# Kernel tuning notes

Measured on AMD Instinct MI355X. Metric: run time of the kernel, lower is better.

## Reference

```python
import jax, jax.numpy as jnp
import numpy as np

N = 8192
F_IN = 512
F_HID = 256
ALPHA = 0.2  # LeakyReLU negative slope
NEG_INF = -9e15


def gat_layer(h, adj, W, a):
    """Standard dense GraphAttentionLayer (pyGAT style).
    h: [N, F_in], adj: [N, N] (0/1), W: [F_in, F_out], a: [2*F_out, 1].
    """
    Wh = h @ W  # [N, F_out]
    f_out = W.shape[1]
    # e_ij = leakyrelu(a1 . Wh_i + a2 . Wh_j) via broadcasting
    e1 = Wh @ a[:f_out]      # [N, 1]
    e2 = Wh @ a[f_out:]      # [N, 1]
    e = jax.nn.leaky_relu(e1 + e2.T, negative_slope=ALPHA)  # [N, N]
    e = jnp.where(adj > 0, e, NEG_INF)
    att = jax.nn.softmax(e, axis=-1)  # masked row softmax
    return jax.nn.elu(att @ Wh)       # [N, F_out]


def setup_inputs() -> dict:
    key = jax.random.key(0)
    k_x, k_adj, k_w1, k_a1, k_w2, k_a2 = jax.random.split(key, 6)
    x = jax.random.normal(k_x, (N, F_IN), dtype=jnp.float32)
    # sparse random adjacency (~avg degree 16) + self loops
    adj = (jax.random.uniform(k_adj, (N, N)) < (16.0 / N)).astype(jnp.float32)
    adj = jnp.clip(adj + jnp.eye(N, dtype=jnp.float32), 0.0, 1.0)
    # Xavier-ish init for layer params
    W1 = jax.random.normal(k_w1, (F_IN, F_HID), dtype=jnp.float32) * (1.0 / np.sqrt(F_IN))
    a1 = jax.random.normal(k_a1, (2 * F_HID, 1), dtype=jnp.float32) * (1.0 / np.sqrt(2 * F_HID))
    W2 = jax.random.normal(k_w2, (F_HID, F_IN), dtype=jnp.float32) * (1.0 / np.sqrt(F_HID))
    a2 = jax.random.normal(k_a2, (2 * F_IN, 1), dtype=jnp.float32) * (1.0 / np.sqrt(2 * F_IN))
    return {"x": x, "adj": adj, "W1": W1, "a1": a1, "W2": W2, "a2": a2}


def reference(x, adj, W1, a1, W2, a2):
    enc = gat_layer(x, adj, W1, a1)    # encode: [N, F_HID]
    dec = gat_layer(enc, adj, W2, a2)  # decode: [N, F_IN]
    return (dec, enc)
```

## Files before the change

### kernel.cpp

```cpp
#include <hip/hip_runtime.h>
#include <hip/hip_bf16.h>

#define N_NODES 8192
#define F_IN    512
#define F_HID   256
#define ALPHA   0.2f
#define MAXDEG  64

using f32x4 = __attribute__((ext_vector_type(4))) float;
using f16x8 = __attribute__((ext_vector_type(8))) _Float16;
using f16x4 = __attribute__((ext_vector_type(4))) _Float16;

__global__ void prep_kernel(const float* __restrict__ W1, const float* __restrict__ W2,
                            _Float16* __restrict__ W1T, _Float16* __restrict__ W2T,
                            const float* __restrict__ a2,
                            float* __restrict__ w2s, float* __restrict__ w2t,
                            float* __restrict__ stz) {
    const int tid = threadIdx.x;
    int gid = blockIdx.x * 256 + tid;
    if (gid < 2 * N_NODES) stz[gid] = 0.0f;

    if (blockIdx.x >= 256) {
        const int r = (blockIdx.x - 256) * 64 + (tid >> 2);
        const int q = tid & 3;
        float ss = 0.f, tt = 0.f;
        for (int n = q * 4; n < F_IN; n += 16) {
            f32x4 w  = *(const f32x4*)&W2[(size_t)r * F_IN + n];
            f32x4 as = *(const f32x4*)&a2[n];
            f32x4 at = *(const f32x4*)&a2[F_IN + n];
            #pragma unroll
            for (int j = 0; j < 4; ++j) { ss += w[j] * as[j]; tt += w[j] * at[j]; }
        }
        ss += __shfl_xor(ss, 1); ss += __shfl_xor(ss, 2);
        tt += __shfl_xor(tt, 1); tt += __shfl_xor(tt, 2);
        if (q == 0) { w2s[r] = ss; w2t[r] = tt; }
        return;
    }

    int t = blockIdx.x;
    const float* W; _Float16* WT; int K, N, kt, nt;
    if (t < 128) { W = W1; WT = W1T; K = 512; N = 256; kt = t & 15; nt = t >> 4; }
    else { t -= 128; W = W2; WT = W2T; K = 256; N = 512; kt = t & 7; nt = t >> 3; }
    __shared__ float Ws[32][33];
    const int tx = tid & 31, ty = tid >> 5;
    #pragma unroll
    for (int i = 0; i < 4; ++i)
        Ws[ty + 8 * i][tx] = W[(size_t)(kt * 32 + ty + 8 * i) * N + nt * 32 + tx];
    __syncthreads();
    #pragma unroll
    for (int i = 0; i < 4; ++i)
        WT[(size_t)(nt * 32 + ty + 8 * i) * K + kt * 32 + tx] = (_Float16)Ws[tx][ty + 8 * i];
}

__device__ inline int csr_scan(const float* __restrict__ adj, int* __restrict__ crow,
                               int* jLds, int row, int lane) {
    const f32x4* arow = (const f32x4*)(adj + (size_t)row * N_NODES);
    int count = 0;
    const unsigned long long mlt = (1ULL << lane) - 1ULL;
    for (int base = 0; base < N_NODES; base += 512) {
        f32x4 v0 = __builtin_nontemporal_load(&arow[(base >> 2) + lane]);
        f32x4 v1 = __builtin_nontemporal_load(&arow[(base >> 2) + 64 + lane]);
        unsigned long long b0 = __ballot(v0[0] > 0.0f);
        unsigned long long b1 = __ballot(v0[1] > 0.0f);
        unsigned long long b2 = __ballot(v0[2] > 0.0f);
        unsigned long long b3 = __ballot(v0[3] > 0.0f);
        unsigned long long b4 = __ballot(v1[0] > 0.0f);
        unsigned long long b5 = __ballot(v1[1] > 0.0f);
        unsigned long long b6 = __ballot(v1[2] > 0.0f);
        unsigned long long b7 = __ballot(v1[3] > 0.0f);
        int o = count + __popcll(b0 & mlt) + __popcll(b1 & mlt)
                      + __popcll(b2 & mlt) + __popcll(b3 & mlt);
        int c0 = base + (lane << 2);
        if (v0[0] > 0.0f) { if (o < MAXDEG) { crow[o] = c0;     if (jLds) jLds[o] = c0;     } o++; }
        if (v0[1] > 0.0f) { if (o < MAXDEG) { crow[o] = c0 + 1; if (jLds) jLds[o] = c0 + 1; } o++; }
        if (v0[2] > 0.0f) { if (o < MAXDEG) { crow[o] = c0 + 2; if (jLds) jLds[o] = c0 + 2; } o++; }
        if (v0[3] > 0.0f) { if (o < MAXDEG) { crow[o] = c0 + 3; if (jLds) jLds[o] = c0 + 3; } o++; }
        count += __popcll(b0) + __popcll(b1) + __popcll(b2) + __popcll(b3);
        o = count + __popcll(b4 & mlt) + __popcll(b5 & mlt)
                  + __popcll(b6 & mlt) + __popcll(b7 & mlt);
        int c1 = base + 256 + (lane << 2);
        if (v1[0] > 0.0f) { if (o < MAXDEG) { crow[o] = c1;     if (jLds) jLds[o] = c1;     } o++; }
        if (v1[1] > 0.0f) { if (o < MAXDEG) { crow[o] = c1 + 1; if (jLds) jLds[o] = c1 + 1; } o++; }
        if (v1[2] > 0.0f) { if (o < MAXDEG) { crow[o] = c1 + 2; if (jLds) jLds[o] = c1 + 2; } o++; }
        if (v1[3] > 0.0f) { if (o < MAXDEG) { crow[o] = c1 + 3; if (jLds) jLds[o] = c1 + 3; } o++; }
        count += __popcll(b4) + __popcll(b5) + __popcll(b6) + __popcll(b7);
    }
    return count > MAXDEG ? MAXDEG : count;
}

__device__ inline void gemm1_tile(const float* __restrict__ x,
                                  const _Float16* __restrict__ W1T,
                                  _Float16* __restrict__ Wh1,
                                  const float* __restrict__ a1,
                                  float* __restrict__ s1, float* __restrict__ t1,
                                  int brow, int bcol) {
    const int LDT = 72;
    __shared__ _Float16 As[64 * LDT];
    __shared__ _Float16 Bs[128 * LDT];
    const int tid = threadIdx.x;
    const int wid = tid >> 6, lane = tid & 63;
    const int wr = (wid >> 1) * 32, wc = (wid & 1) * 64;
    const int sr = tid >> 3, skg = (tid & 7) * 8;

    f32x4 acc[2][4];
    #pragma unroll
    for (int m = 0; m < 2; ++m)
        #pragma unroll
        for (int n = 0; n < 4; ++n) acc[m][n] = f32x4{0.f, 0.f, 0.f, 0.f};

    for (int k0 = 0; k0 < F_IN; k0 += 64) {
        #pragma unroll
        for (int i = 0; i < 2; ++i) {
            int r = sr + i * 32;
            const f32x4* src = (const f32x4*)(x + (size_t)(brow + r) * F_IN + k0 + skg);
            f32x4 a0 = src[0];
            f32x4 a1v = src[1];
            f16x8 av;
            #pragma unroll
            for (int j = 0; j < 4; ++j) { av[j] = (_Float16)a0[j]; av[4 + j] = (_Float16)a1v[j]; }
            *(f16x8*)&As[r * LDT + skg] = av;
        }
        #pragma unroll
        for (int i = 0; i < 4; ++i) {
            int r = sr + i * 32;
            *(f16x8*)&Bs[r * LDT + skg] =
                *(const f16x8*)&W1T[(size_t)(bcol + r) * F_IN + k0 + skg];
        }
        __syncthreads();
        #pragma unroll
        for (int ks = 0; ks < 2; ++ks) {
            const int kb = ks * 32 + (lane >> 4) * 8;
            f16x8 af[2], bfr[4];
            #pragma unroll
            for (int m = 0; m < 2; ++m)
                af[m] = *(const f16x8*)&As[(wr + m * 16 + (lane & 15)) * LDT + kb];
            #pragma unroll
            for (int n = 0; n < 4; ++n)
                bfr[n] = *(const f16x8*)&Bs[(wc + n * 16 + (lane & 15)) * LDT + kb];
            #pragma unroll
            for (int m = 0; m < 2; ++m)
                #pragma unroll
                for (int n = 0; n < 4; ++n)
                    acc[m][n] = __builtin_amdgcn_mfma_f32_16x16x32_f16(
                        af[m], bfr[n], acc[m][n], 0, 0, 0);
        }
        __syncthreads();
    }
    const int cl = lane & 15;
    float as[4], at[4];
    #pragma unroll
    for (int n = 0; n < 4; ++n) {
        as[n] = a1[bcol + wc + n * 16 + cl];
        at[n] = a1[F_HID + bcol + wc + n * 16 + cl];
    }
    #pragma unroll
    for (int m = 0; m < 2; ++m) {
        #pragma unroll
        for (int j = 0; j < 4; ++j) {
            float vs = 0.f, vt = 0.f;
            #pragma unroll
            for (int n = 0; n < 4; ++n) { vs += acc[m][n][j] * as[n]; vt += acc[m][n][j] * at[n]; }
            #pragma unroll
            for (int off = 1; off < 16; off <<= 1) {
                vs += __shfl_xor(vs, off);
                vt += __shfl_xor(vt, off);
            }
            if (cl == 0) {
                int row = brow + wr + m * 16 + ((lane >> 4) << 2) + j;
                atomicAdd(s1 + row, vs);
                atomicAdd(t1 + row, vt);
            }
        }
        #pragma unroll
        for (int n = 0; n < 4; ++n) {
            int row = brow + wr + m * 16 + ((lane >> 4) << 2);
            int col = bcol + wc + n * 16 + cl;
            #pragma unroll
            for (int j = 0; j < 4; ++j)
                Wh1[(size_t)(row + j) * F_HID + col] = (_Float16)acc[m][n][j];
        }
    }
}

__global__ __launch_bounds__(256)
void gemm1_csr(const float* __restrict__ adj, int* __restrict__ cols,
               int* __restrict__ cnt, const float* __restrict__ x,
               const _Float16* __restrict__ W1T, _Float16* __restrict__ Wh1,
               const float* __restrict__ a1,
               float* __restrict__ s1, float* __restrict__ t1) {
    const int bid = blockIdx.x;
    const int g = bid / 5, r = bid % 5;
    if (r == 0) {
        gemm1_tile(x, W1T, Wh1, a1, s1, t1, (g & 127) * 64, (g >> 7) * 128);
    } else {
        const int q = g * 4 + (r - 1);
        const int row = q * 4 + (threadIdx.x >> 6);
        const int lane = threadIdx.x & 63;
        int deg = csr_scan(adj, cols + (size_t)row * MAXDEG, nullptr, row, lane);
        if (lane == 0) cnt[row] = deg;
    }
}

__global__ __launch_bounds__(256)
void csr_agg1(const float* __restrict__ adj, int* __restrict__ cols,
              int* __restrict__ cnt, const _Float16* __restrict__ Wh1,
              const float* __restrict__ s1, const float* __restrict__ t1,
              const float* __restrict__ w2s, const float* __restrict__ w2t,
              float* __restrict__ enc, _Float16* __restrict__ enc16,
              float* __restrict__ s2, float* __restrict__ t2) {
    const int bid = blockIdx.x;
    const int wid = threadIdx.x >> 6, lane = threadIdx.x & 63;
    const bool doCsr = !(bid & 1);
    const int quad = doCsr ? 1024 + (bid >> 1) : (bid >> 1);
    const int row = quad * 4 + wid;
    __shared__ int jS[4][64];
    __shared__ float pS[4][64];

    int deg;
    if (doCsr) {
        deg = csr_scan(adj, cols + (size_t)row * MAXDEG, jS[wid], row, lane);
        if (lane == 0) cnt[row] = deg;
    } else {
        deg = cnt[row];
        if (lane < deg) jS[wid][lane] = cols[(size_t)row * MAXDEG + lane];
    }

    const float sI = s1[row];
    float ev = -1e30f;
    if (lane < deg) {
        float z = sI + t1[jS[wid][lane]];
        ev = z > 0.0f ? z : ALPHA * z;
    }
    float m = ev;
    #pragma unroll
    for (int off = 32; off > 0; off >>= 1) m = fmaxf(m, __shfl_xor(m, off));
    float ex = (lane < deg) ? __expf(ev - m) : 0.0f;
    float sum = ex;
    #pragma unroll
    for (int off = 32; off > 0; off >>= 1) sum += __shfl_xor(sum, off);
    pS[wid][lane] = ex / sum;

    float acc[4] = {};
    const size_t lo = (size_t)lane * 4;
    int d = 0;
    for (; d + 4 <= deg; d += 4) {
        float p0 = pS[wid][d],     p1 = pS[wid][d + 1];
        float p2 = pS[wid][d + 2], p3 = pS[wid][d + 3];
        f16x4 v0 = *(const f16x4*)(Wh1 + (size_t)jS[wid][d] * F_HID + lo);
        f16x4 v1 = *(const f16x4*)(Wh1 + (size_t)jS[wid][d + 1] * F_HID + lo);
        f16x4 v2 = *(const f16x4*)(Wh1 + (size_t)jS[wid][d + 2] * F_HID + lo);
        f16x4 v3 = *(const f16x4*)(Wh1 + (size_t)jS[wid][d + 3] * F_HID + lo);
        #pragma unroll
        for (int jj = 0; jj < 4; ++jj)
            acc[jj] += p0 * (float)v0[jj] + p1 * (float)v1[jj]
                     + p2 * (float)v2[jj] + p3 * (float)v3[jj];
    }
    for (; d < deg; ++d) {
        float p = pS[wid][d];
        f16x4 w = *(const f16x4*)(Wh1 + (size_t)jS[wid][d] * F_HID + lo);
        #pragma unroll
        for (int jj = 0; jj < 4; ++jj) acc[jj] += p * (float)w[jj];
    }
    f32x4 o; f16x4 h;
    #pragma unroll
    for (int jj = 0; jj < 4; ++jj) {
        float v = acc[jj];
        float e = v > 0.0f ? v : (__expf(v) - 1.0f);
        o[jj] = e; h[jj] = (_Float16)e;
    }
    __builtin_nontemporal_store(o, (f32x4*)(enc + (size_t)row * F_HID + lo));
    *(f16x4*)(enc16 + (size_t)row * F_HID + lo) = h;

    f32x4 ws = *(const f32x4*)(w2s + lo);
    f32x4 wt = *(const f32x4*)(w2t + lo);
    float ps = 0.f, pt = 0.f;
    #pragma unroll
    for (int jj = 0; jj < 4; ++jj) { ps += o[jj] * ws[jj]; pt += o[jj] * wt[jj]; }
    #pragma unroll
    for (int off = 32; off > 0; off >>= 1) {
        ps += __shfl_xor(ps, off);
        pt += __shfl_xor(pt, off);
    }
    if (lane == 0) { s2[row] = ps; t2[row] = pt; }
}

__global__ __launch_bounds__(256)
void l2_fused(const _Float16* __restrict__ enc16, const _Float16* __restrict__ W2T,
              const int* __restrict__ cols, const int* __restrict__ cnt,
              const float* __restrict__ s2, const float* __restrict__ t2,
              float* __restrict__ dec) {
    const int LDA = 264, LDB = 264;
    __shared__ _Float16 aggE[16 * LDA];
    __shared__ _Float16 Bs[64 * LDB];
    const int base = blockIdx.x * 16;
    const int wid = threadIdx.x >> 6, lane = threadIdx.x & 63;

    for (int rr = 0; rr < 4; ++rr) {
        const int row = base + wid * 4 + rr;
        const int deg = cnt[row];
        const float sI = s2[row];
        int j = 0;
        float ev = -1e30f;
        if (lane < deg) {
            j = cols[(size_t)row * MAXDEG + lane];
            float z = sI + t2[j];
            ev = z > 0.0f ? z : ALPHA * z;
        }
        float m = ev;
        #pragma unroll
        for (int off = 32; off > 0; off >>= 1) m = fmaxf(m, __shfl_xor(m, off));
        float ex = (lane < deg) ? __expf(ev - m) : 0.0f;
        float sum = ex;
        #pragma unroll
        for (int off = 32; off > 0; off >>= 1) sum += __shfl_xor(sum, off);
        float p = ex / sum;

        float acc[4] = {};
        const size_t lo = (size_t)lane * 4;
        int d = 0;
        for (; d + 4 <= deg; d += 4) {
            float p0 = __shfl(p, d),     p1 = __shfl(p, d + 1);
            float p2 = __shfl(p, d + 2), p3 = __shfl(p, d + 3);
            int j0 = __shfl(j, d),     j1 = __shfl(j, d + 1);
            int j2 = __shfl(j, d + 2), j3 = __shfl(j, d + 3);
            f16x4 v0 = *(const f16x4*)(enc16 + (size_t)j0 * F_HID + lo);
            f16x4 v1 = *(const f16x4*)(enc16 + (size_t)j1 * F_HID + lo);
            f16x4 v2 = *(const f16x4*)(enc16 + (size_t)j2 * F_HID + lo);
            f16x4 v3 = *(const f16x4*)(enc16 + (size_t)j3 * F_HID + lo);
            #pragma unroll
            for (int jj = 0; jj < 4; ++jj)
                acc[jj] += p0 * (float)v0[jj] + p1 * (float)v1[jj]
                         + p2 * (float)v2[jj] + p3 * (float)v3[jj];
        }
        for (; d < deg; ++d) {
            float pd = __shfl(p, d);
            int jd = __shfl(j, d);
            f16x4 v = *(const f16x4*)(enc16 + (size_t)jd * F_HID + lo);
            #pragma unroll
            for (int jj = 0; jj < 4; ++jj) acc[jj] += pd * (float)v[jj];
        }
        f16x4 h;
        #pragma unroll
        for (int jj = 0; jj < 4; ++jj) h[jj] = (_Float16)acc[jj];
        *(f16x4*)&aggE[(wid * 4 + rr) * LDA + lane * 4] = h;
    }
    __syncthreads();

    f16x8 af[8];
    #pragma unroll
    for (int kf = 0; kf < 8; ++kf)
        af[kf] = *(const f16x8*)&aggE[(lane & 15) * LDA + kf * 32 + (lane >> 4) * 8];

    for (int ct = 0; ct < 8; ++ct) {
        #pragma unroll
        for (int i = 0; i < 8; ++i) {
            int idx = threadIdx.x + i * 256;
            int c = idx >> 5, kg = (idx & 31) * 8;
            *(f16x8*)&Bs[c * LDB + kg] =
                *(const f16x8*)&W2T[(size_t)(ct * 64 + c) * F_HID + kg];
        }
        __syncthreads();
        f32x4 oacc = f32x4{0.f, 0.f, 0.f, 0.f};
        #pragma unroll
        for (int kf = 0; kf < 8; ++kf) {
            f16x8 bf = *(const f16x8*)&Bs[(wid * 16 + (lane & 15)) * LDB
                                          + kf * 32 + (lane >> 4) * 8];
            oacc = __builtin_amdgcn_mfma_f32_16x16x32_f16(af[kf], bf, oacc, 0, 0, 0);
        }
        const int col = ct * 64 + wid * 16 + (lane & 15);
        const int row0 = base + ((lane >> 4) << 2);
        #pragma unroll
        for (int jj = 0; jj < 4; ++jj) {
            float v = oacc[jj];
            float e = v > 0.0f ? v : (__expf(v) - 1.0f);
            __builtin_nontemporal_store(e, &dec[(size_t)(row0 + jj) * F_IN + col]);
        }
        __syncthreads();
    }
}

extern "C" void kernel_launch(void* const* d_in, const int* in_sizes, int n_in,
                              void* d_out, int out_size, void* d_ws, size_t ws_size,
                              hipStream_t stream) {
    (void)in_sizes; (void)n_in; (void)out_size; (void)ws_size;
    const float* x   = (const float*)d_in[0];
    const float* adj = (const float*)d_in[1];
    const float* W1  = (const float*)d_in[2];
    const float* a1  = (const float*)d_in[3];
    const float* W2  = (const float*)d_in[4];
    const float* a2  = (const float*)d_in[5];

    float* dec = (float*)d_out;
    float* enc = dec + (size_t)N_NODES * F_IN;

    int*      cols  = (int*)d_ws;
    int*      cnt   = cols + (size_t)N_NODES * MAXDEG;
    float*    s1    = (float*)(cnt + N_NODES);
    float*    t1    = s1 + N_NODES;
    float*    s2    = t1 + N_NODES;
    float*    t2    = s2 + N_NODES;
    float*    w2s   = t2 + N_NODES;
    float*    w2t   = w2s + F_HID;
    _Float16* Wh1   = (_Float16*)(w2t + F_HID);
    _Float16* enc16 = Wh1 + (size_t)N_NODES * F_HID;
    _Float16* W1T   = enc16 + (size_t)N_NODES * F_HID;
    _Float16* W2T   = W1T + (size_t)F_HID * F_IN;

    prep_kernel<<<260, 256, 0, stream>>>(W1, W2, W1T, W2T, a2, w2s, w2t, s1);

    gemm1_csr<<<1280, 256, 0, stream>>>(adj, cols, cnt, x, W1T, Wh1, a1, s1, t1);

    csr_agg1<<<2048, 256, 0, stream>>>(adj, cols, cnt, Wh1, s1, t1,
                                       w2s, w2t, enc, enc16, s2, t2);

    l2_fused<<<N_NODES / 16, 256, 0, stream>>>(enc16, W2T, cols, cnt, s2, t2, dec);
}
```

Baseline: 120.0 us.

## Move all CSR scanning into GEMM1 kernel and use half-wave 8-wide gathers

All adjacency scanning now happens in the combined first kernel: 256 GEMM blocks plus 2048 CSR blocks, up from half the rows before. The aggregation kernel becomes a pure gather/softmax pass. Both aggregation loops now split each wave into two halves that process alternate neighbors with 16-byte f16x8 loads, then combine the halves with a cross-half shuffle. This rebalances the big 256 MB adjacency read so it overlaps with the GEMM rather than delaying aggregation, at the cost of a larger first kernel and extra shuffle reductions.

```diff
diff --git a/kernel.cpp b/kernel.cpp
--- a/kernel.cpp
+++ b/kernel.cpp
@@ -52,9 +52,10 @@
         WT[(size_t)(nt * 32 + ty + 8 * i) * K + kt * 32 + tx] = (_Float16)Ws[tx][ty + 8 * i];
 }
 
-__device__ inline int csr_scan(const float* __restrict__ adj, int* __restrict__ crow,
-                               int* jLds, int row, int lane) {
+__device__ inline void csr_row(const float* __restrict__ adj, int* __restrict__ cols,
+                               int* __restrict__ cnt, int row, int lane) {
     const f32x4* arow = (const f32x4*)(adj + (size_t)row * N_NODES);
+    int* crow = cols + (size_t)row * MAXDEG;
     int count = 0;
     const unsigned long long mlt = (1ULL << lane) - 1ULL;
     for (int base = 0; base < N_NODES; base += 512) {
@@ -71,21 +72,21 @@
         int o = count + __popcll(b0 & mlt) + __popcll(b1 & mlt)
                       + __popcll(b2 & mlt) + __popcll(b3 & mlt);
         int c0 = base + (lane << 2);
-        if (v0[0] > 0.0f) { if (o < MAXDEG) { crow[o] = c0;     if (jLds) jLds[o] = c0;     } o++; }
-        if (v0[1] > 0.0f) { if (o < MAXDEG) { crow[o] = c0 + 1; if (jLds) jLds[o] = c0 + 1; } o++; }
-        if (v0[2] > 0.0f) { if (o < MAXDEG) { crow[o] = c0 + 2; if (jLds) jLds[o] = c0 + 2; } o++; }
-        if (v0[3] > 0.0f) { if (o < MAXDEG) { crow[o] = c0 + 3; if (jLds) jLds[o] = c0 + 3; } o++; }
+        if (v0[0] > 0.0f) { if (o < MAXDEG) crow[o] = c0;     o++; }
+        if (v0[1] > 0.0f) { if (o < MAXDEG) crow[o] = c0 + 1; o++; }
+        if (v0[2] > 0.0f) { if (o < MAXDEG) crow[o] = c0 + 2; o++; }
+        if (v0[3] > 0.0f) { if (o < MAXDEG) crow[o] = c0 + 3; o++; }
         count += __popcll(b0) + __popcll(b1) + __popcll(b2) + __popcll(b3);
         o = count + __popcll(b4 & mlt) + __popcll(b5 & mlt)
                   + __popcll(b6 & mlt) + __popcll(b7 & mlt);
         int c1 = base + 256 + (lane << 2);
-        if (v1[0] > 0.0f) { if (o < MAXDEG) { crow[o] = c1;     if (jLds) jLds[o] = c1;     } o++; }
-        if (v1[1] > 0.0f) { if (o < MAXDEG) { crow[o] = c1 + 1; if (jLds) jLds[o] = c1 + 1; } o++; }
-        if (v1[2] > 0.0f) { if (o < MAXDEG) { crow[o] = c1 + 2; if (jLds) jLds[o] = c1 + 2; } o++; }
-        if (v1[3] > 0.0f) { if (o < MAXDEG) { crow[o] = c1 + 3; if (jLds) jLds[o] = c1 + 3; } o++; }
+        if (v1[0] > 0.0f) { if (o < MAXDEG) crow[o] = c1;     o++; }
+        if (v1[1] > 0.0f) { if (o < MAXDEG) crow[o] = c1 + 1; o++; }
+        if (v1[2] > 0.0f) { if (o < MAXDEG) crow[o] = c1 + 2; o++; }
+        if (v1[3] > 0.0f) { if (o < MAXDEG) crow[o] = c1 + 3; o++; }
         count += __popcll(b4) + __popcll(b5) + __popcll(b6) + __popcll(b7);
     }
-    return count > MAXDEG ? MAXDEG : count;
+    if (lane == 0) cnt[row] = count > MAXDEG ? MAXDEG : count;
 }
 
 __device__ inline void gemm1_tile(const float* __restrict__ x,
@@ -183,52 +184,38 @@
 }
 
 __global__ __launch_bounds__(256)
-void gemm1_csr(const float* __restrict__ adj, int* __restrict__ cols,
-               int* __restrict__ cnt, const float* __restrict__ x,
-               const _Float16* __restrict__ W1T, _Float16* __restrict__ Wh1,
-               const float* __restrict__ a1,
-               float* __restrict__ s1, float* __restrict__ t1) {
+void csr_and_gemm1(const float* __restrict__ adj, int* __restrict__ cols,
+                   int* __restrict__ cnt, const float* __restrict__ x,
+                   const _Float16* __restrict__ W1T, _Float16* __restrict__ Wh1,
+                   const float* __restrict__ a1,
+                   float* __restrict__ s1, float* __restrict__ t1) {
     const int bid = blockIdx.x;
-    const int g = bid / 5, r = bid % 5;
-    if (r == 0) {
-        gemm1_tile(x, W1T, Wh1, a1, s1, t1, (g & 127) * 64, (g >> 7) * 128);
+    if (bid < 256) {
+        gemm1_tile(x, W1T, Wh1, a1, s1, t1, (bid & 127) * 64, (bid >> 7) * 128);
     } else {
-        const int q = g * 4 + (r - 1);
+        const int q = bid - 256;
         const int row = q * 4 + (threadIdx.x >> 6);
-        const int lane = threadIdx.x & 63;
-        int deg = csr_scan(adj, cols + (size_t)row * MAXDEG, nullptr, row, lane);
-        if (lane == 0) cnt[row] = deg;
+        csr_row(adj, cols, cnt, row, threadIdx.x & 63);
     }
 }
 
 __global__ __launch_bounds__(256)
-void csr_agg1(const float* __restrict__ adj, int* __restrict__ cols,
-              int* __restrict__ cnt, const _Float16* __restrict__ Wh1,
-              const float* __restrict__ s1, const float* __restrict__ t1,
-              const float* __restrict__ w2s, const float* __restrict__ w2t,
-              float* __restrict__ enc, _Float16* __restrict__ enc16,
-              float* __restrict__ s2, float* __restrict__ t2) {
-    const int bid = blockIdx.x;
+void aggregate_l1(const _Float16* __restrict__ Wh,
+                  const int* __restrict__ cols, const int* __restrict__ cnt,
+                  const float* __restrict__ s, const float* __restrict__ t,
+                  const float* __restrict__ w2s, const float* __restrict__ w2t,
+                  float* __restrict__ enc, _Float16* __restrict__ enc16,
+                  float* __restrict__ s2, float* __restrict__ t2) {
     const int wid = threadIdx.x >> 6, lane = threadIdx.x & 63;
-    const bool doCsr = !(bid & 1);
-    const int quad = doCsr ? 1024 + (bid >> 1) : (bid >> 1);
-    const int row = quad * 4 + wid;
-    __shared__ int jS[4][64];
-    __shared__ float pS[4][64];
-
-    int deg;
-    if (doCsr) {
-        deg = csr_scan(adj, cols + (size_t)row * MAXDEG, jS[wid], row, lane);
-        if (lane == 0) cnt[row] = deg;
-    } else {
-        deg = cnt[row];
-        if (lane < deg) jS[wid][lane] = cols[(size_t)row * MAXDEG + lane];
-    }
-
-    const float sI = s1[row];
+    const int row = blockIdx.x * 4 + wid;
+    const int deg = cnt[row];
+    const int half = lane >> 5, fl = lane & 31;
+
+    int j = 0;
     float ev = -1e30f;
     if (lane < deg) {
-        float z = sI + t1[jS[wid][lane]];
+        j = cols[(size_t)row * MAXDEG + lane];
+        float z = s[row] + t[j];
         ev = z > 0.0f ? z : ALPHA * z;
     }
     float m = ev;
@@ -238,46 +225,57 @@
     float sum = ex;
     #pragma unroll
     for (int off = 32; off > 0; off >>= 1) sum += __shfl_xor(sum, off);
-    pS[wid][lane] = ex / sum;
-
-    float acc[4] = {};
-    const size_t lo = (size_t)lane * 4;
+    const float pp = ex / sum;
+
+    float acc[8] = {};
+    const size_t fo = (size_t)fl * 8;
     int d = 0;
-    for (; d + 4 <= deg; d += 4) {
-        float p0 = pS[wid][d],     p1 = pS[wid][d + 1];
-        float p2 = pS[wid][d + 2], p3 = pS[wid][d + 3];
-        f16x4 v0 = *(const f16x4*)(Wh1 + (size_t)jS[wid][d] * F_HID + lo);
-        f16x4 v1 = *(const f16x4*)(Wh1 + (size_t)jS[wid][d + 1] * F_HID + lo);
-        f16x4 v2 = *(const f16x4*)(Wh1 + (size_t)jS[wid][d + 2] * F_HID + lo);
-        f16x4 v3 = *(const f16x4*)(Wh1 + (size_t)jS[wid][d + 3] * F_HID + lo);
-        #pragma unroll
-        for (int jj = 0; jj < 4; ++jj)
-            acc[jj] += p0 * (float)v0[jj] + p1 * (float)v1[jj]
-                     + p2 * (float)v2[jj] + p3 * (float)v3[jj];
-    }
-    for (; d < deg; ++d) {
-        float p = pS[wid][d];
-        f16x4 w = *(const f16x4*)(Wh1 + (size_t)jS[wid][d] * F_HID + lo);
-        #pragma unroll
-        for (int jj = 0; jj < 4; ++jj) acc[jj] += p * (float)w[jj];
-    }
-    f32x4 o; f16x4 h;
-    #pragma unroll
-    for (int jj = 0; jj < 4; ++jj) {
-        float v = acc[jj];
-        float e = v > 0.0f ? v : (__expf(v) - 1.0f);
-        o[jj] = e; h[jj] = (_Float16)e;
-    }
-    __builtin_nontemporal_store(o, (f32x4*)(enc + (size_t)row * F_HID + lo));
-    *(f16x4*)(enc16 + (size_t)row * F_HID + lo) = h;
-
-    f32x4 ws = *(const f32x4*)(w2s + lo);
-    f32x4 wt = *(const f32x4*)(w2t + lo);
+    for (; d + 2 <= deg; d += 2) {
+        const int dd = d + half;
+        float pd = __shfl(pp, dd);
+        int jd = __shfl(j, dd);
+        f16x8 v = *(const f16x8*)(Wh + (size_t)jd * F_HID + fo);
+        #pragma unroll
+        for (int k = 0; k < 8; ++k) acc[k] += pd * (float)v[k];
+    }
+    if (deg & 1) {
+        const int dd = deg - 1;
+        float pd = __shfl(pp, dd);
+        int jd = __shfl(j, dd);
+        if (half == 0) {
+            f16x8 v = *(const f16x8*)(Wh + (size_t)jd * F_HID + fo);
+            #pragma unroll
+            for (int k = 0; k < 8; ++k) acc[k] += pd * (float)v[k];
+        }
+    }
+    #pragma unroll
+    for (int k = 0; k < 8; ++k) acc[k] += __shfl_xor(acc[k], 32);
+
     float ps = 0.f, pt = 0.f;
-    #pragma unroll
-    for (int jj = 0; jj < 4; ++jj) { ps += o[jj] * ws[jj]; pt += o[jj] * wt[jj]; }
-    #pragma unroll
-    for (int off = 32; off > 0; off >>= 1) {
+    if (half == 0) {
+        f32x4 o0, o1; f16x8 h;
+        #pragma unroll
+        for (int k = 0; k < 8; ++k) {
+            float v = acc[k];
+            float e = v > 0.0f ? v : (__expf(v) - 1.0f);
+            if (k < 4) o0[k] = e; else o1[k - 4] = e;
+            h[k] = (_Float16)e;
+            acc[k] = e;
+        }
+        __builtin_nontemporal_store(o0, (f32x4*)(enc + (size_t)row * F_HID + fo));
+        __builtin_nontemporal_store(o1, (f32x4*)(enc + (size_t)row * F_HID + fo + 4));
+        *(f16x8*)(enc16 + (size_t)row * F_HID + fo) = h;
+
+        f32x4 ws0 = *(const f32x4*)(w2s + fo), ws1 = *(const f32x4*)(w2s + fo + 4);
+        f32x4 wt0 = *(const f32x4*)(w2t + fo), wt1 = *(const f32x4*)(w2t + fo + 4);
+        #pragma unroll
+        for (int k = 0; k < 4; ++k) {
+            ps += acc[k] * ws0[k] + acc[k + 4] * ws1[k];
+            pt += acc[k] * wt0[k] + acc[k + 4] * wt1[k];
+        }
+    }
+    #pragma unroll
+    for (int off = 16; off > 0; off >>= 1) {
         ps += __shfl_xor(ps, off);
         pt += __shfl_xor(pt, off);
     }
@@ -294,6 +292,7 @@
     __shared__ _Float16 Bs[64 * LDB];
     const int base = blockIdx.x * 16;
     const int wid = threadIdx.x >> 6, lane = threadIdx.x & 63;
+    const int half = lane >> 5, fl = lane & 31;
 
     for (int rr = 0; rr < 4; ++rr) {
         const int row = base + wid * 4 + rr;
@@ -313,36 +312,37 @@
         float sum = ex;
         #pragma unroll
         for (int off = 32; off > 0; off >>= 1) sum += __shfl_xor(sum, off);
-        float p = ex / sum;
-
-        float acc[4] = {};
-        const size_t lo = (size_t)lane * 4;
+        const float pp = ex / sum;
+
+        float acc[8] = {};
+        const size_t fo = (size_t)fl * 8;
         int d = 0;
-        for (; d + 4 <= deg; d += 4) {
-            float p0 = __shfl(p, d),     p1 = __shfl(p, d + 1);
-            float p2 = __shfl(p, d + 2), p3 = __shfl(p, d + 3);
-            int j0 = __shfl(j, d),     j1 = __shfl(j, d + 1);
-            int j2 = __shfl(j, d + 2), j3 = __shfl(j, d + 3);
-            f16x4 v0 = *(const f16x4*)(enc16 + (size_t)j0 * F_HID + lo);
-            f16x4 v1 = *(const f16x4*)(enc16 + (size_t)j1 * F_HID + lo);
-            f16x4 v2 = *(const f16x4*)(enc16 + (size_t)j2 * F_HID + lo);
-            f16x4 v3 = *(const f16x4*)(enc16 + (size_t)j3 * F_HID + lo);
-            #pragma unroll
-            for (int jj = 0; jj < 4; ++jj)
-                acc[jj] += p0 * (float)v0[jj] + p1 * (float)v1[jj]
-                         + p2 * (float)v2[jj] + p3 * (float)v3[jj];
-        }
-        for (; d < deg; ++d) {
-            float pd = __shfl(p, d);
-            int jd = __shfl(j, d);
-            f16x4 v = *(const f16x4*)(enc16 + (size_t)jd * F_HID + lo);
-            #pragma unroll
-            for (int jj = 0; jj < 4; ++jj) acc[jj] += pd * (float)v[jj];
-        }
-        f16x4 h;
-        #pragma unroll
-        for (int jj = 0; jj < 4; ++jj) h[jj] = (_Float16)acc[jj];
-        *(f16x4*)&aggE[(wid * 4 + rr) * LDA + lane * 4] = h;
+        for (; d + 2 <= deg; d += 2) {
+            const int dd = d + half;
+            float pd = __shfl(pp, dd);
+            int jd = __shfl(j, dd);
+            f16x8 v = *(const f16x8*)(enc16 + (size_t)jd * F_HID + fo);
+            #pragma unroll
+            for (int k = 0; k < 8; ++k) acc[k] += pd * (float)v[k];
+        }
+        if (deg & 1) {
+            const int dd = deg - 1;
+            float pd = __shfl(pp, dd);
+            int jd = __shfl(j, dd);
+            if (half == 0) {
+                f16x8 v = *(const f16x8*)(enc16 + (size_t)jd * F_HID + fo);
+                #pragma unroll
+                for (int k = 0; k < 8; ++k) acc[k] += pd * (float)v[k];
+            }
+        }
+        #pragma unroll
+        for (int k = 0; k < 8; ++k) acc[k] += __shfl_xor(acc[k], 32);
+        if (half == 0) {
+            f16x8 h;
+            #pragma unroll
+            for (int k = 0; k < 8; ++k) h[k] = (_Float16)acc[k];
+            *(f16x8*)&aggE[(wid * 4 + rr) * LDA + fl * 8] = h;
+        }
     }
     __syncthreads();
 
@@ -408,10 +408,10 @@
 
     prep_kernel<<<260, 256, 0, stream>>>(W1, W2, W1T, W2T, a2, w2s, w2t, s1);
 
-    gemm1_csr<<<1280, 256, 0, stream>>>(adj, cols, cnt, x, W1T, Wh1, a1, s1, t1);
-
-    csr_agg1<<<2048, 256, 0, stream>>>(adj, cols, cnt, Wh1, s1, t1,
-                                       w2s, w2t, enc, enc16, s2, t2);
+    csr_and_gemm1<<<2304, 256, 0, stream>>>(adj, cols, cnt, x, W1T, Wh1, a1, s1, t1);
+
+    aggregate_l1<<<N_NODES / 4, 256, 0, stream>>>(Wh1, cols, cnt, s1, t1,
+                                                  w2s, w2t, enc, enc16, s2, t2);
 
     l2_fused<<<N_NODES / 16, 256, 0, stream>>>(enc16, W2T, cols, cnt, s2, t2, dec);
 }
```

New measurement: 108.8 us. -9.4%, faster.
